# Optimization experiments

Measured on AMD Instinct MI355X. Metric: run time of the kernel, lower is better.

Reference implementation:

```python
import jax, jax.numpy as jnp
import numpy as np

N_NODES = 100000
N_EDGES = 1600000
HIDDEN = 64
EPS = 1e-5


def setup_inputs() -> dict:
    key = jax.random.key(0)
    ks = jax.random.split(key, 12)
    h = HIDDEN
    inp = {
        'x': jax.random.normal(ks[0], (N_NODES, h), dtype=jnp.float32),
        'edge_index': jax.random.randint(ks[1], (2, N_EDGES), 0, N_NODES, dtype=jnp.int32),
        'message': jax.random.normal(ks[2], (N_EDGES, h), dtype=jnp.float32),
        # node_mlp: Linear(2h->h), BN(h), ReLU, Dropout(identity), Linear(h->h), BN(h), ReLU
        'W1': jax.random.normal(ks[3], (2 * h, h), dtype=jnp.float32) / np.sqrt(2.0 * h),
        'b1': jnp.zeros((h,), jnp.float32),
        'g1': jnp.ones((h,), jnp.float32),
        'be1': jnp.zeros((h,), jnp.float32),
        'W2': jax.random.normal(ks[4], (h, h), dtype=jnp.float32) / np.sqrt(h),
        'b2': jnp.zeros((h,), jnp.float32),
        'g2': jnp.ones((h,), jnp.float32),
        'be2': jnp.zeros((h,), jnp.float32),
        # attention_mlp: Linear(h->1), Sigmoid
        'Wa': jax.random.normal(ks[5], (h, 1), dtype=jnp.float32) / np.sqrt(h),
        'ba': jnp.zeros((1,), jnp.float32),
    }
    return inp


def _scatter_max(msg, idx, n):
    # torch_scatter scatter(..., reduce='max') fills segments with no edges with 0
    agg = jax.ops.segment_max(msg, idx, num_segments=n)  # [N, H], -inf where empty
    cnt = jax.ops.segment_sum(jnp.ones((idx.shape[0],), msg.dtype), idx, num_segments=n)
    return jnp.where(cnt[:, None] > 0, agg, jnp.zeros((), msg.dtype))


def _batchnorm(x, gamma, beta):
    # training-mode BatchNorm1d: batch mean / biased variance
    mu = jnp.mean(x, axis=0)
    var = jnp.mean((x - mu) ** 2, axis=0)
    return (x - mu) * jax.lax.rsqrt(var + EPS) * gamma + beta


def reference(x, edge_index, message, W1, b1, g1, be1, W2, b2, g2, be2, Wa, ba):
    n = x.shape[0]
    row, col = edge_index[0], edge_index[1]
    fwd = _scatter_max(message, col, n)   # [N, H]
    bwd = _scatter_max(message, row, n)   # [N, H]
    out = jnp.concatenate([fwd, bwd], axis=1)          # [N, 2H]
    h1 = jax.nn.relu(_batchnorm(out @ W1 + b1, g1, be1))  # dropout = identity (eval)
    h2 = jax.nn.relu(_batchnorm(h1 @ W2 + b2, g2, be2))   # [N, H]
    att = jax.nn.sigmoid(h2 @ Wa + ba).reshape(-1)          # [N]
    return (h2, att)
```

## Files before the change

kernel.cpp:

```cpp
#include <hip/hip_runtime.h>
#include <hip/hip_bf16.h>
#include <cstdint>
#include <cstddef>

#define HDIM 64
#define EPS 1e-5f
#define BN 64
#define BSH 6
#define LR 65
#define NXCD 8
#define BCAPX 256
#define CURPAD 16
#define SENTE 64u

typedef short bf16x8 __attribute__((ext_vector_type(8)));
typedef float f32x4  __attribute__((ext_vector_type(4)));
typedef float f4v    __attribute__((ext_vector_type(4)));
typedef unsigned u2v __attribute__((ext_vector_type(2)));

__device__ __forceinline__ unsigned bf16rn(float f) {
    unsigned u = __float_as_uint(f);
    return (u + 0x7FFFu + ((u >> 16) & 1u)) >> 16;
}

__global__ __launch_bounds__(256) void bucket_fill_kernel(
    const int* __restrict__ ei, unsigned* __restrict__ bcur,
    unsigned* __restrict__ entries, int E, int nblk) {
    int e = blockIdx.x * 256 + threadIdx.x;
    if (e >= E) return;
    unsigned xcd;
    asm volatile("s_getreg_b32 %0, hwreg(HW_REG_XCC_ID)" : "=s"(xcd));
    xcd &= (NXCD - 1);
    int row = ei[e];
    int col = ei[(size_t)E + e];
    unsigned cell1 = (unsigned)(col >> BSH) * NXCD + xcd;
    unsigned cell2 = (unsigned)(nblk + (row >> BSH)) * NXCD + xcd;
    unsigned p1 = atomicAdd(&bcur[(size_t)cell1 * CURPAD], 1u);
    unsigned p2 = atomicAdd(&bcur[(size_t)cell2 * CURPAD], 1u);
    if (p1 < BCAPX)
        entries[(size_t)cell1 * BCAPX + p1] = ((unsigned)e << 7) | (unsigned)(col & (BN - 1));
    if (p2 < BCAPX)
        entries[(size_t)cell2 * BCAPX + p2] = ((unsigned)e << 7) | (unsigned)(row & (BN - 1));
}

__global__ __launch_bounds__(256) void binned_max_kernel(
    const float* __restrict__ msg, const unsigned* __restrict__ bcur,
    const unsigned* __restrict__ entries,
    unsigned short* __restrict__ fwdB, unsigned short* __restrict__ bwdB,
    int N, int nblk) {
    __shared__ __align__(16) float acc[4 * LR * BN];
    int tid = threadIdx.x;
    int wave = tid >> 6, lane = tid & 63;
    int b = blockIdx.x;

    {
        f4v mi = { -INFINITY, -INFINITY, -INFINITY, -INFINITY };
        f4v* p = (f4v*)acc;
        for (int i = tid; i < 4 * LR * BN / 4; i += 256) p[i] = mi;
    }
    __syncthreads();
    float* accw = acc + wave * (LR * BN);

    for (int rr = 0; rr < 2; ++rr) {
        int r = wave + rr * 4;
        unsigned cnt = bcur[((size_t)b * NXCD + r) * CURPAD];
        if (cnt > BCAPX) cnt = BCAPX;
        const unsigned* rb = entries + ((size_t)b * NXCD + r) * BCAPX;
        for (unsigned c0 = 0; c0 < cnt; c0 += 64) {
            unsigned myent = (c0 + (unsigned)lane < cnt) ? rb[c0 + lane] : SENTE;
            unsigned rem = cnt - c0;
            float v[16];
#pragma unroll
            for (int k = 0; k < 16; ++k) {
                unsigned ent = __shfl(myent, k);
                v[k] = __builtin_nontemporal_load(&msg[(size_t)(ent >> 7) * HDIM + lane]);
            }
#pragma unroll
            for (int b16 = 0; b16 < 4; ++b16) {
                if ((unsigned)(b16 * 16) >= rem) break;
                bool more = (unsigned)((b16 + 1) * 16) < rem;
                float vn[16];
                if (more) {
#pragma unroll
                    for (int k = 0; k < 16; ++k) {
                        unsigned ent = __shfl(myent, (b16 + 1) * 16 + k);
                        vn[k] = __builtin_nontemporal_load(&msg[(size_t)(ent >> 7) * HDIM + lane]);
                    }
                }
#pragma unroll
                for (int k = 0; k < 16; ++k) {
                    unsigned ent = __shfl(myent, b16 * 16 + k);
                    unsigned sl = ent & 127u;
                    float* a = &accw[sl * BN + lane];
                    *a = fmaxf(*a, v[k]);
                }
                if (more) {
#pragma unroll
                    for (int k = 0; k < 16; ++k) v[k] = vn[k];
                }
            }
        }
    }
    __syncthreads();

    bool fwd = (b < nblk);
    int node0 = (fwd ? b : b - nblk) * BN;
    unsigned short* dst = fwd ? fwdB : bwdB;
    for (int i = tid; i < BN * (HDIM / 4); i += 256) {
        int rrow = i >> 4, c4 = (i & 15) * 4;
        int node = node0 + rrow;
        if (node >= N) continue;
        int off = rrow * HDIM + c4;
        f4v m0 = *(const f4v*)&acc[0 * LR * BN + off];
        f4v m1 = *(const f4v*)&acc[1 * LR * BN + off];
        f4v m2 = *(const f4v*)&acc[2 * LR * BN + off];
        f4v m3 = *(const f4v*)&acc[3 * LR * BN + off];
        f4v m;
#pragma unroll
        for (int k = 0; k < 4; ++k) {
            float x = fmaxf(fmaxf(m0[k], m1[k]), fmaxf(m2[k], m3[k]));
            m[k] = (x == -INFINITY) ? 0.0f : x;
        }
        u2v o;
        o.x = bf16rn(m[0]) | (bf16rn(m[1]) << 16);
        o.y = bf16rn(m[2]) | (bf16rn(m[3]) << 16);
        *(u2v*)(dst + (size_t)node * HDIM + c4) = o;
    }
}


__global__ __launch_bounds__(256) void prep_w_kernel(
    const float* __restrict__ W1, const float* __restrict__ W2,
    unsigned short* __restrict__ W1T, unsigned short* __restrict__ W2T) {
    int t = blockIdx.x * 256 + threadIdx.x;
    if (t < 128 * 64) {
        int k = t >> 6, o = t & 63;
        W1T[o * 128 + k] = (unsigned short)bf16rn(W1[t]);
    } else {
        int t2 = t - 128 * 64;
        if (t2 < 64 * 64) {
            int k = t2 >> 6, o = t2 & 63;
            W2T[o * 64 + k] = (unsigned short)bf16rn(W2[t2]);
        }
    }
}

__global__ __launch_bounds__(256) void gemm1_mfma_kernel(
    const unsigned short* __restrict__ fwdB, const unsigned short* __restrict__ bwdB,
    const unsigned short* __restrict__ W1T, const float* __restrict__ b1,
    float* __restrict__ y1, float* __restrict__ sum1, float* __restrict__ sq1, int N) {
    __shared__ float wsum[4][64], wsq[4][64];
    int tid = threadIdx.x;
    int wave = tid >> 6, lane = tid & 63;
    int lrow = lane & 15, kseg = lane >> 4;
    int rbase = blockIdx.x * 64 + wave * 16;

    bf16x8 bfr[4][4];
#pragma unroll
    for (int nt = 0; nt < 4; ++nt)
#pragma unroll
        for (int kb = 0; kb < 4; ++kb)
            bfr[nt][kb] = *(const bf16x8*)(W1T + (size_t)(nt * 16 + lrow) * 128 + kb * 32 + kseg * 8);

    int r = rbase + lrow;
    bool ok = (r < N);
    size_t ro = (size_t)(ok ? r : 0) * HDIM;
    bf16x8 z = {};
    bf16x8 afr[4];
    afr[0] = *(const bf16x8*)(fwdB + ro + kseg * 8);
    afr[1] = *(const bf16x8*)(fwdB + ro + 32 + kseg * 8);
    afr[2] = *(const bf16x8*)(bwdB + ro + kseg * 8);
    afr[3] = *(const bf16x8*)(bwdB + ro + 32 + kseg * 8);
    if (!ok) { afr[0] = z; afr[1] = z; afr[2] = z; afr[3] = z; }

    f32x4 acc[4] = {};
#pragma unroll
    for (int kb = 0; kb < 4; ++kb)
#pragma unroll
        for (int nt = 0; nt < 4; ++nt)
            acc[nt] = __builtin_amdgcn_mfma_f32_16x16x32_bf16(afr[kb], bfr[nt][kb], acc[nt], 0, 0, 0);

#pragma unroll
    for (int nt = 0; nt < 4; ++nt) {
        int col = nt * 16 + lrow;
        float bias = b1[col];
        float s = 0.f, q = 0.f;
#pragma unroll
        for (int rr = 0; rr < 4; ++rr) {
            int rowi = rbase + kseg * 4 + rr;
            if (rowi < N) {
                float v = acc[nt][rr] + bias;
                y1[(size_t)rowi * HDIM + col] = v;
                s += v; q += v * v;
            }
        }
        s += __shfl_xor(s, 16); s += __shfl_xor(s, 32);
        q += __shfl_xor(q, 16); q += __shfl_xor(q, 32);
        if (kseg == 0) { wsum[wave][col] = s; wsq[wave][col] = q; }
    }
    __syncthreads();
    if (tid < 64) {
        float S = wsum[0][tid] + wsum[1][tid] + wsum[2][tid] + wsum[3][tid];
        float Q = wsq[0][tid] + wsq[1][tid] + wsq[2][tid] + wsq[3][tid];
        atomicAdd(&sum1[tid], S);
        atomicAdd(&sq1[tid], Q);
    }
}

__global__ __launch_bounds__(256) void gemm2_mfma_kernel(
    const float* __restrict__ y1, const float* __restrict__ sum1, const float* __restrict__ sq1,
    const float* __restrict__ g1, const float* __restrict__ be1,
    const unsigned short* __restrict__ W2T, const float* __restrict__ b2,
    float* __restrict__ y2, float* __restrict__ sum2, float* __restrict__ sq2, int N) {
    __shared__ float sc[64], sh[64];
    __shared__ float wsum[4][64], wsq[4][64];
    int tid = threadIdx.x;
    if (tid < 64) {
        float invN = 1.0f / (float)N;
        float mu = sum1[tid] * invN;
        float var = sq1[tid] * invN - mu * mu;
        float rs = rsqrtf(var + EPS);
        float s = rs * g1[tid];
        sc[tid] = s;
        sh[tid] = be1[tid] - mu * s;
    }
    __syncthreads();
    int wave = tid >> 6, lane = tid & 63;
    int lrow = lane & 15, kseg = lane >> 4;
    int rbase = blockIdx.x * 64 + wave * 16;

    bf16x8 bfr[4][2];
#pragma unroll
    for (int nt = 0; nt < 4; ++nt)
#pragma unroll
        for (int kb = 0; kb < 2; ++kb)
            bfr[nt][kb] = *(const bf16x8*)(W2T + (size_t)(nt * 16 + lrow) * 64 + kb * 32 + kseg * 8);

    int r = rbase + lrow;
    size_t ro = (size_t)((r < N) ? r : 0) * HDIM;
    bf16x8 afr[2];
#pragma unroll
    for (int kb = 0; kb < 2; ++kb) {
        const f4v* yp = (const f4v*)(y1 + ro + kb * 32 + kseg * 8);
        f4v u0 = yp[0], u1 = yp[1];
        int k0 = kb * 32 + kseg * 8;
        bf16x8 a;
#pragma unroll
        for (int j = 0; j < 4; ++j) {
            float h0 = fmaxf(fmaf(u0[j], sc[k0 + j], sh[k0 + j]), 0.f);
            float h1 = fmaxf(fmaf(u1[j], sc[k0 + 4 + j], sh[k0 + 4 + j]), 0.f);
            a[j] = (short)bf16rn(h0);
            a[4 + j] = (short)bf16rn(h1);
        }
        afr[kb] = a;
    }

    f32x4 acc[4] = {};
#pragma unroll
    for (int kb = 0; kb < 2; ++kb)
#pragma unroll
        for (int nt = 0; nt < 4; ++nt)
            acc[nt] = __builtin_amdgcn_mfma_f32_16x16x32_bf16(afr[kb], bfr[nt][kb], acc[nt], 0, 0, 0);

#pragma unroll
    for (int nt = 0; nt < 4; ++nt) {
        int col = nt * 16 + lrow;
        float bias = b2[col];
        float s = 0.f, q = 0.f;
#pragma unroll
        for (int rr = 0; rr < 4; ++rr) {
            int rowi = rbase + kseg * 4 + rr;
            if (rowi < N) {
                float v = acc[nt][rr] + bias;
                y2[(size_t)rowi * HDIM + col] = v;
                s += v; q += v * v;
            }
        }
        s += __shfl_xor(s, 16); s += __shfl_xor(s, 32);
        q += __shfl_xor(q, 16); q += __shfl_xor(q, 32);
        if (kseg == 0) { wsum[wave][col] = s; wsq[wave][col] = q; }
    }
    __syncthreads();
    if (tid < 64) {
        float S = wsum[0][tid] + wsum[1][tid] + wsum[2][tid] + wsum[3][tid];
        float Q = wsq[0][tid] + wsq[1][tid] + wsq[2][tid] + wsq[3][tid];
        atomicAdd(&sum2[tid], S);
        atomicAdd(&sq2[tid], Q);
    }
}

__global__ __launch_bounds__(256) void final_kernel(
    const float* __restrict__ y2, const float* __restrict__ sum2, const float* __restrict__ sq2,
    const float* __restrict__ g2, const float* __restrict__ be2,
    const float* __restrict__ Wa, const float* __restrict__ ba,
    float* __restrict__ out_h2, float* __restrict__ out_att, int N) {
    __shared__ float sc[HDIM], sh[HDIM], wa[HDIM];
    __shared__ float bav;
    if (threadIdx.x < HDIM) {
        int c = threadIdx.x;
        float invN = 1.0f / (float)N;
        float mu = sum2[c] * invN;
        float var = sq2[c] * invN - mu * mu;
        float rstd = rsqrtf(var + EPS);
        float s = rstd * g2[c];
        sc[c] = s;
        sh[c] = be2[c] - mu * s;
        wa[c] = Wa[c];
    }
    if (threadIdx.x == 0) bav = ba[0];
    __syncthreads();
    int n = blockIdx.x * 256 + threadIdx.x;
    if (n >= N) return;

    const f4v* p = (const f4v*)&y2[(size_t)n * HDIM];
    f4v* dst = (f4v*)&out_h2[(size_t)n * HDIM];
    float att = bav;
#pragma unroll 1
    for (int kk = 0; kk < 16; ++kk) {
        f4v u = p[kk];
        f4v hv;
#pragma unroll
        for (int j = 0; j < 4; ++j) {
            int k = kk * 4 + j;
            float h = fmaxf(fmaf(u[j], sc[k], sh[k]), 0.0f);
            hv[j] = h;
            att = fmaf(h, wa[k], att);
        }
        dst[kk] = hv;
    }
    out_att[n] = 1.0f / (1.0f + expf(-att));
}

extern "C" void kernel_launch(void* const* d_in, const int* in_sizes, int n_in,
                              void* d_out, int out_size, void* d_ws, size_t ws_size,
                              hipStream_t stream) {
    const int*   ei   = (const int*)d_in[1];
    const float* msg  = (const float*)d_in[2];
    const float* W1   = (const float*)d_in[3];
    const float* b1   = (const float*)d_in[4];
    const float* g1   = (const float*)d_in[5];
    const float* be1  = (const float*)d_in[6];
    const float* W2   = (const float*)d_in[7];
    const float* b2   = (const float*)d_in[8];
    const float* g2   = (const float*)d_in[9];
    const float* be2  = (const float*)d_in[10];
    const float* Wa   = (const float*)d_in[11];
    const float* ba   = (const float*)d_in[12];

    const int N = in_sizes[0] / HDIM;
    const int E = in_sizes[1] / 2;
    const int nblk = (N + BN - 1) / BN;

    unsigned short* fwdB = (unsigned short*)d_ws;
    unsigned short* bwdB = fwdB + (size_t)N * HDIM;
    unsigned short* W1T  = bwdB + (size_t)N * HDIM;
    unsigned short* W2T  = W1T + 8192;
    float*    stats      = (float*)(W2T + 4096);
    unsigned* bcur       = (unsigned*)(stats + 256);
    unsigned* entries    = bcur + (size_t)2 * nblk * NXCD * CURPAD;
    float*    y1         = (float*)d_out;
    float*    y2         = (float*)d_ws;
    float*    out_att    = (float*)d_out + (size_t)N * HDIM;

    hipMemsetAsync(stats, 0, 256 * sizeof(float)
                             + (size_t)2 * nblk * NXCD * CURPAD * sizeof(unsigned), stream);
    prep_w_kernel<<<48, 256, 0, stream>>>(W1, W2, W1T, W2T);

    int eblocks = (E + 255) / 256;
    bucket_fill_kernel<<<eblocks, 256, 0, stream>>>(ei, bcur, entries, E, nblk);
    binned_max_kernel<<<2 * nblk, 256, 0, stream>>>(msg, bcur, entries, fwdB, bwdB, N, nblk);

    int G = (N + 63) / 64;
    gemm1_mfma_kernel<<<G, 256, 0, stream>>>(fwdB, bwdB, W1T, b1, y1,
                                             stats, stats + 64, N);
    gemm2_mfma_kernel<<<G, 256, 0, stream>>>(y1, stats, stats + 64, g1, be1,
                                             W2T, b2, y2, stats + 128, stats + 192, N);
    final_kernel<<<(N + 255) / 256, 256, 0, stream>>>(y2, stats + 128, stats + 192,
                                                      g2, be2, Wa, ba,
                                                      (float*)d_out, out_att, N);
}
```

Before: 498.5 us.

## Use shared LDS atomic max on order-flipped floats with larger node bins

Replaces the four per-wave private float accumulators with one block-shared accumulator updated by ds_max_u32 on sign-flipped float bits, using a sentinel for empty rows. This allows the bin size to double to 128 nodes and raises per-cell bucket capacity, so far fewer blocks and less LDS init and reduction work are needed per node. The software prefetch of the next message batch is dropped, which may expose gather latency. LDS atomics can also contend when many edges hit the same node.

Measured after the change: 429.9 us. 13.8% less time.

```diff
diff --git a/kernel.cpp b/kernel.cpp
--- a/kernel.cpp
+++ b/kernel.cpp
@@ -5,13 +5,13 @@
 
 #define HDIM 64
 #define EPS 1e-5f
-#define BN 64
-#define BSH 6
-#define LR 65
+#define BN 128
+#define BSH 7
 #define NXCD 8
-#define BCAPX 256
+#define BCAPX 2560
 #define CURPAD 16
-#define SENTE 64u
+#define SENTE 128u
+static const unsigned SENT = 0x007FFFFFu;
 
 typedef short bf16x8 __attribute__((ext_vector_type(8)));
 typedef float f32x4  __attribute__((ext_vector_type(4)));
@@ -21,6 +21,17 @@
 __device__ __forceinline__ unsigned bf16rn(float f) {
     unsigned u = __float_as_uint(f);
     return (u + 0x7FFFu + ((u >> 16) & 1u)) >> 16;
+}
+
+__device__ __forceinline__ unsigned flipf(float f) {
+    unsigned u = __float_as_uint(f);
+    return u ^ (((unsigned)((int)u >> 31)) | 0x80000000u);
+}
+
+__device__ __forceinline__ float unflip(unsigned u) {
+    if (u == SENT) return 0.0f;
+    unsigned b = (u & 0x80000000u) ? (u & 0x7FFFFFFFu) : ~u;
+    return __uint_as_float(b);
 }
 
 __global__ __launch_bounds__(256) void bucket_fill_kernel(
@@ -38,9 +49,9 @@
     unsigned p1 = atomicAdd(&bcur[(size_t)cell1 * CURPAD], 1u);
     unsigned p2 = atomicAdd(&bcur[(size_t)cell2 * CURPAD], 1u);
     if (p1 < BCAPX)
-        entries[(size_t)cell1 * BCAPX + p1] = ((unsigned)e << 7) | (unsigned)(col & (BN - 1));
+        entries[(size_t)cell1 * BCAPX + p1] = ((unsigned)e << 8) | (unsigned)(col & (BN - 1));
     if (p2 < BCAPX)
-        entries[(size_t)cell2 * BCAPX + p2] = ((unsigned)e << 7) | (unsigned)(row & (BN - 1));
+        entries[(size_t)cell2 * BCAPX + p2] = ((unsigned)e << 8) | (unsigned)(row & (BN - 1));
 }
 
 __global__ __launch_bounds__(256) void binned_max_kernel(
@@ -48,18 +59,20 @@
     const unsigned* __restrict__ entries,
     unsigned short* __restrict__ fwdB, unsigned short* __restrict__ bwdB,
     int N, int nblk) {
-    __shared__ __align__(16) float acc[4 * LR * BN];
+    __shared__ __align__(16) unsigned acc[(BN + 1) * HDIM];
     int tid = threadIdx.x;
     int wave = tid >> 6, lane = tid & 63;
     int b = blockIdx.x;
 
     {
-        f4v mi = { -INFINITY, -INFINITY, -INFINITY, -INFINITY };
-        f4v* p = (f4v*)acc;
-        for (int i = tid; i < 4 * LR * BN / 4; i += 256) p[i] = mi;
-    }
-    __syncthreads();
-    float* accw = acc + wave * (LR * BN);
+        uint4 sv; sv.x = SENT; sv.y = SENT; sv.z = SENT; sv.w = SENT;
+        uint4* p = (uint4*)acc;
+        for (int i = tid; i < (BN + 1) * HDIM / 4; i += 256) p[i] = sv;
+    }
+    __syncthreads();
+
+    unsigned accBase = (unsigned)(size_t)&acc[0];
+    unsigned laneOff = accBase + ((unsigned)lane << 2);
 
     for (int rr = 0; rr < 2; ++rr) {
         int r = wave + rr * 4;
@@ -69,38 +82,25 @@
         for (unsigned c0 = 0; c0 < cnt; c0 += 64) {
             unsigned myent = (c0 + (unsigned)lane < cnt) ? rb[c0 + lane] : SENTE;
             unsigned rem = cnt - c0;
-            float v[16];
-#pragma unroll
-            for (int k = 0; k < 16; ++k) {
-                unsigned ent = __shfl(myent, k);
-                v[k] = __builtin_nontemporal_load(&msg[(size_t)(ent >> 7) * HDIM + lane]);
-            }
 #pragma unroll
             for (int b16 = 0; b16 < 4; ++b16) {
                 if ((unsigned)(b16 * 16) >= rem) break;
-                bool more = (unsigned)((b16 + 1) * 16) < rem;
-                float vn[16];
-                if (more) {
-#pragma unroll
-                    for (int k = 0; k < 16; ++k) {
-                        unsigned ent = __shfl(myent, (b16 + 1) * 16 + k);
-                        vn[k] = __builtin_nontemporal_load(&msg[(size_t)(ent >> 7) * HDIM + lane]);
-                    }
-                }
+                float v[16];
 #pragma unroll
                 for (int k = 0; k < 16; ++k) {
                     unsigned ent = __shfl(myent, b16 * 16 + k);
-                    unsigned sl = ent & 127u;
-                    float* a = &accw[sl * BN + lane];
-                    *a = fmaxf(*a, v[k]);
+                    v[k] = __builtin_nontemporal_load(&msg[(size_t)(ent >> 8) * HDIM + lane]);
                 }
-                if (more) {
-#pragma unroll
-                    for (int k = 0; k < 16; ++k) v[k] = vn[k];
+#pragma unroll
+                for (int k = 0; k < 16; ++k) {
+                    unsigned ent = __shfl(myent, b16 * 16 + k);
+                    unsigned addr = laneOff + ((ent & 255u) << 8);
+                    asm volatile("ds_max_u32 %0, %1" :: "v"(addr), "v"(flipf(v[k])));
                 }
             }
         }
     }
+    asm volatile("" ::: "memory");
     __syncthreads();
 
     bool fwd = (b < nblk);
@@ -110,20 +110,12 @@
         int rrow = i >> 4, c4 = (i & 15) * 4;
         int node = node0 + rrow;
         if (node >= N) continue;
-        int off = rrow * HDIM + c4;
-        f4v m0 = *(const f4v*)&acc[0 * LR * BN + off];
-        f4v m1 = *(const f4v*)&acc[1 * LR * BN + off];
-        f4v m2 = *(const f4v*)&acc[2 * LR * BN + off];
-        f4v m3 = *(const f4v*)&acc[3 * LR * BN + off];
-        f4v m;
-#pragma unroll
-        for (int k = 0; k < 4; ++k) {
-            float x = fmaxf(fmaxf(m0[k], m1[k]), fmaxf(m2[k], m3[k]));
-            m[k] = (x == -INFINITY) ? 0.0f : x;
-        }
+        uint4 a = *(const uint4*)&acc[rrow * HDIM + c4];
+        float v0 = unflip(a.x), v1 = unflip(a.y);
+        float v2 = unflip(a.z), v3 = unflip(a.w);
         u2v o;
-        o.x = bf16rn(m[0]) | (bf16rn(m[1]) << 16);
-        o.y = bf16rn(m[2]) | (bf16rn(m[3]) << 16);
+        o.x = bf16rn(v0) | (bf16rn(v1) << 16);
+        o.y = bf16rn(v2) | (bf16rn(v3) << 16);
         *(u2v*)(dst + (size_t)node * HDIM + c4) = o;
     }
 }
```
